# Performance work log

Measured on AMD Instinct MI355X. Metric: run time of the kernel, lower is better.

The kernel has to match this reference:

```python
import jax, jax.numpy as jnp
import numpy as np

N_BASIS = 5  # identity, transpose, diag-embed(diag), row-sum broadcast, total-sum broadcast


def eq2to2_ops(x):
    """x: [B, d, n, n] -> [B, 5, d, n, n] equivariant basis ops (sums normalized by n, n^2)."""
    n = x.shape[-1]
    eye = jnp.eye(n, dtype=x.dtype)
    xt = jnp.swapaxes(x, -1, -2)
    diag = jnp.diagonal(x, axis1=-2, axis2=-1)            # [B, d, n]
    diag_emb = diag[..., :, None] * eye                   # [B, d, n, n]
    row = jnp.broadcast_to(x.sum(-1, keepdims=True) / n, x.shape)
    tot = jnp.broadcast_to(x.sum((-2, -1), keepdims=True) / (n * n), x.shape)
    return jnp.stack([x, xt, diag_emb, row, tot], axis=1)


def eq_layer(x, W, b):
    """x: [B, d_in, n, n]; W: [d_in, d_out, 5]; b: [d_out] -> [B, d_out, n, n]."""
    ops = eq2to2_ops(x)                                   # [B, 5, d_in, n, n]
    return jnp.einsum('bqdij,dsq->bsij', ops, W) + b[None, :, None, None]


def setup_inputs() -> dict:
    key = jax.random.key(0)
    ks = jax.random.split(key, 8)
    B, n, nin, nhid, ndechid, nout = 8, 256, 16, 32, 128, 1
    s = lambda fan: 1.0 / np.sqrt(fan)
    return {
        'x': jax.random.normal(ks[0], (B, n, nin), jnp.float32),
        'W1': jax.random.normal(ks[1], (2 * nin, nhid, N_BASIS), jnp.float32) * s(2 * nin * N_BASIS),
        'b1': jnp.zeros((nhid,), jnp.float32),
        'W2': jax.random.normal(ks[2], (nhid, nhid, N_BASIS), jnp.float32) * s(nhid * N_BASIS),
        'b2': jnp.zeros((nhid,), jnp.float32),
        'D1': jax.random.normal(ks[3], (nhid, ndechid), jnp.float32) * s(nhid),
        'db1': jnp.zeros((ndechid,), jnp.float32),
        'D2': jax.random.normal(ks[4], (ndechid, ndechid), jnp.float32) * s(ndechid),
        'db2': jnp.zeros((ndechid,), jnp.float32),
        'D3': jax.random.normal(ks[5], (ndechid, nout), jnp.float32) * s(ndechid),
        'db3': jnp.zeros((nout,), jnp.float32),
    }


def reference(x, W1, b1, W2, b2, D1, db1, D2, db2, D3, db3):
    B, n, d = x.shape
    eye = jnp.eye(n, dtype=x.dtype)
    # diag_embed(x.permute(0,2,1)) -> [B, d, n, n]
    x1 = jnp.swapaxes(x, 1, 2)[..., :, None] * eye
    # outer-product pairwise interactions -> [B, d, n, n]
    x2 = jnp.einsum('bid,bjd->bdij', x, x)
    h = jnp.concatenate([x1, x2], axis=1)                 # [B, 2d, n, n]
    h = jax.nn.relu(eq_layer(h, W1, b1))
    h = jax.nn.relu(eq_layer(h, W2, b2))
    h = jax.nn.relu(h.sum((-2, -1)))                      # [B, nhid]
    h = jax.nn.relu(h @ D1 + db1)
    h = jax.nn.relu(h @ D2 + db2)
    return h @ D3 + db3
```

## Files before the change

### kernel.cpp

```cpp
#include <hip/hip_runtime.h>
#include <hip/hip_bf16.h>


#define NB 8
#define NN 256
#define ND 16
#define NC 32
#define W1S 160
#define W2S 160

using bf16x8 = __attribute__((ext_vector_type(8))) __bf16;
using f32x4  = __attribute__((ext_vector_type(4))) float;

#define MFMA(a, b, c) __builtin_amdgcn_mfma_f32_16x16x32_bf16((a), (b), (c), 0, 0, 0)

__global__ __launch_bounds__(256) void kC_rows(
    const float* __restrict__ x, const float* __restrict__ W1,
    const float* __restrict__ b1, const float* __restrict__ W2,
    float* __restrict__ T1g, float* __restrict__ R1, float* __restrict__ Dg1,
    float* __restrict__ TotP, float* __restrict__ CD2, float* __restrict__ CR2)
{
    const int TI = blockIdx.x, b = blockIdx.y, t = threadIdx.x;
    __shared__ __align__(16) float  sX[NN][ND + 1];
    __shared__ __align__(16) __bf16 sP[NN][40];
    __shared__ __align__(16) __bf16 sBQ[NC][48];
    __shared__ float part[16][ND + 1];
    __shared__ float sS[ND], sT1[NC];
    __shared__ float sRT[8][NC], sDgL[8][NC], sRow[8][NC], sDiag[8][NC];

    const float* xg = x + b * NN * ND;
    #pragma unroll
    for (int kk = 0; kk < 16; ++kk) {
        int idx = t + kk * 256;
        sX[idx >> 4][idx & 15] = xg[idx];
    }
    #pragma unroll
    for (int kk = 0; kk < 2; ++kk) {
        int idx = t + kk * 256;
        int c = idx >> 4, k = idx & 15;
        sBQ[c][k] = (__bf16)(W1[(ND + k) * W1S + c * 5 + 0]
                           + W1[(ND + k) * W1S + c * 5 + 1]);
    }
    #pragma unroll
    for (int kk = 0; kk < 4; ++kk) {
        int idx = t + kk * 256;
        sBQ[idx >> 5][16 + (idx & 31)] = (__bf16)0.f;
    }
    {
        uint32_t* z = (uint32_t*)&sP[0][0];
        #pragma unroll
        for (int kk = 0; kk < 8; ++kk) {
            int idx = t + kk * 256;
            z[(idx >> 3) * 20 + 8 + (idx & 7)] = 0u;
        }
    }
    __syncthreads();

    {
        int rr = t >> 4, d = t & 15;
        float p = 0.f;
        #pragma unroll
        for (int k = 0; k < 16; ++k) p += sX[rr + (k << 4)][d];
        part[rr][d] = p;
    }
    __syncthreads();
    if (t < ND) {
        float s = 0.f;
        #pragma unroll
        for (int k = 0; k < 16; ++k) s += part[k][t];
        sS[t] = s;
    }
    __syncthreads();
    if (t < NC) {
        int c = t; float tt = 0.f;
        #pragma unroll
        for (int d = 0; d < ND; ++d)
            tt += sS[d] * W1[d * W1S + c * 5 + 4]
                + sS[d] * sS[d] * W1[(ND + d) * W1S + c * 5 + 4];
        float v = tt * (1.f / 65536.f) + b1[c];
        sT1[c] = v;
        if (TI == 0) T1g[b * NC + c] = v;
    }
    __syncthreads();
    {
        int i_l = t >> 5, c = t & 31;
        int gi = TI * 8 + i_l;
        float r = 0.f, dg = 0.f;
        #pragma unroll
        for (int d = 0; d < ND; ++d) {
            float xi = sX[gi][d];
            const float* wa = W1 + d * W1S + c * 5;
            const float* wb = W1 + (ND + d) * W1S + c * 5;
            r  += xi * wa[3] + xi * sS[d] * wb[3];
            dg += xi * (wa[0] + wa[1] + wa[2]) + xi * xi * wb[2];
        }
        r *= (1.f / 256.f);
        R1[(b * NN + gi) * NC + c] = r;
        Dg1[(b * NN + gi) * NC + c] = dg;
        sRT[i_l][c] = sT1[c] + r;
        sDgL[i_l][c] = dg;
    }

    const int ln = t & 63, wv = t >> 6;
    const int m = ln & 15, quad = ln >> 4;
    bf16x8 bq0 = *(const bf16x8*)&sBQ[m][8 * quad];
    bf16x8 bq1 = *(const bf16x8*)&sBQ[m + 16][8 * quad];
    f32x4 zero = {0.f, 0.f, 0.f, 0.f};
    float rs0[4] = {0.f, 0.f, 0.f, 0.f}, rs1[4] = {0.f, 0.f, 0.f, 0.f};
    const int i_base = TI * 8;

    for (int jg = 0; jg < 8; ++jg) {
        __syncthreads();
        {
            int i_l = t >> 5, j_l = t & 31;
            const float* xi = &sX[i_base + i_l][0];
            const float* xj = &sX[jg * 32 + j_l][0];
            bf16x8 v0, v1;
            #pragma unroll
            for (int d = 0; d < 8; ++d) v0[d] = (__bf16)(xi[d] * xj[d]);
            #pragma unroll
            for (int d = 0; d < 8; ++d) v1[d] = (__bf16)(xi[8 + d] * xj[8 + d]);
            *(bf16x8*)&sP[t][0] = v0;
            *(bf16x8*)&sP[t][8] = v1;
        }
        __syncthreads();
        #pragma unroll
        for (int gg = 0; gg < 4; ++gg) {
            int g = wv * 4 + gg;
            bf16x8 av = *(const bf16x8*)&sP[g * 16 + m][8 * quad];
            f32x4 q0 = MFMA(av, bq0, zero);
            f32x4 q1 = MFMA(av, bq1, zero);
            int i_l = g >> 1;
            int gi = i_base + i_l;
            float rt0 = sRT[i_l][m], rt1 = sRT[i_l][m + 16];
            int jb = jg * 32 + (g & 1) * 16 + quad * 4;
            #pragma unroll
            for (int r = 0; r < 4; ++r) {
                float v0 = q0[r] + rt0, v1 = q1[r] + rt1;
                bool dgf = (jb + r == gi);
                if (dgf) { v0 += sDgL[i_l][m]; v1 += sDgL[i_l][m + 16]; }
                float h0 = fmaxf(v0, 0.f), h1 = fmaxf(v1, 0.f);
                if (dgf) { sDiag[i_l][m] = h0; sDiag[i_l][m + 16] = h1; }
                rs0[gg] += h0; rs1[gg] += h1;
            }
        }
    }
    float a0 = rs0[0] + rs0[1], a1 = rs0[2] + rs0[3];
    float b0 = rs1[0] + rs1[1], b1v = rs1[2] + rs1[3];
    a0 += __shfl_down(a0, 32, 64);  a0 += __shfl_down(a0, 16, 64);
    a1 += __shfl_down(a1, 32, 64);  a1 += __shfl_down(a1, 16, 64);
    b0 += __shfl_down(b0, 32, 64);  b0 += __shfl_down(b0, 16, 64);
    b1v += __shfl_down(b1v, 32, 64); b1v += __shfl_down(b1v, 16, 64);
    __syncthreads();
    if (ln < 16) {
        sRow[wv * 2][ln] = a0;       sRow[wv * 2 + 1][ln] = a1;
        sRow[wv * 2][ln + 16] = b0;  sRow[wv * 2 + 1][ln + 16] = b1v;
    }
    __syncthreads();
    if (t < NC) {
        float s = 0.f;
        #pragma unroll
        for (int i = 0; i < 8; ++i) s += sRow[i][t];
        TotP[TI * (NB * NC) + b * NC + t] = s;
    }
    {
        int i_l = t >> 5, s = t & 31;
        int gi = i_base + i_l;
        float cd = 0.f, cr = 0.f;
        #pragma unroll
        for (int c = 0; c < NC; ++c) {
            cd += sDiag[i_l][c] * W2[c * W2S + s * 5 + 2];
            cr += sRow[i_l][c]  * W2[c * W2S + s * 5 + 3];
        }
        CD2[(b * NN + gi) * NC + s] = cd;
        CR2[(b * NN + gi) * NC + s] = cr * (1.f / 256.f);
    }
}

__global__ __launch_bounds__(256) void kD_main(
    const float* __restrict__ x, const float* __restrict__ W1,
    const float* __restrict__ W2, const float* __restrict__ b2,
    const float* __restrict__ T1g, const float* __restrict__ R1g,
    const float* __restrict__ Dg1g, const float* __restrict__ CD2g,
    const float* __restrict__ CR2g, const float* __restrict__ TotP,
    float* __restrict__ GP)
{
    const int b = blockIdx.y, t = threadIdx.x;
    int TI = 0, rem = blockIdx.x;
    while (rem >= 16 - TI) { rem -= 16 - TI; ++TI; }
    const int TJ = TI + rem;
    const bool diagblk = (TI == TJ), mirror = !diagblk;

    __shared__ __align__(16) __bf16 sPA[NN][40];
    __shared__ __align__(16) __bf16 sV[NN][40];
    __shared__ __align__(16) __bf16 sBQ[NC][48];
    __shared__ __align__(16) __bf16 sWp[NC][40];
    __shared__ __align__(16) __bf16 sWm[NC][40];
    __shared__ float sXI[16][ND + 1], sXJ[16][ND + 1];
    __shared__ float sR1I[16][NC], sR1J[16][NC];
    __shared__ float sCR2I[16][NC], sCR2J[16][NC];
    __shared__ float sCD2I[16][NC], sDgI[16][NC];
    __shared__ float sT1[NC], sTot[NC], sCT2[NC];
    __shared__ float red[4][NC];

    { int r = t >> 4, d = t & 15;
      sXI[r][d] = x[(b * NN + TI * 16 + r) * ND + d];
      sXJ[r][d] = x[(b * NN + TJ * 16 + r) * ND + d]; }
    #pragma unroll
    for (int kk = 0; kk < 2; ++kk) {
      int idx = t + kk * 256; int r = idx >> 5, c = idx & 31;
      sR1I[r][c]  = R1g [(b * NN + TI * 16 + r) * NC + c];
      sR1J[r][c]  = R1g [(b * NN + TJ * 16 + r) * NC + c];
      sCR2I[r][c] = CR2g[(b * NN + TI * 16 + r) * NC + c];
      sCR2J[r][c] = CR2g[(b * NN + TJ * 16 + r) * NC + c];
      sCD2I[r][c] = CD2g[(b * NN + TI * 16 + r) * NC + c];
      sDgI[r][c]  = Dg1g[(b * NN + TI * 16 + r) * NC + c];
    }
    #pragma unroll
    for (int kk = 0; kk < 2; ++kk) {
      int idx = t + kk * 256; int c = idx >> 4, k = idx & 15;
      sBQ[c][k] = (__bf16)(W1[(ND + k) * W1S + c * 5 + 0]
                         + W1[(ND + k) * W1S + c * 5 + 1]);
    }
    #pragma unroll
    for (int kk = 0; kk < 4; ++kk) {
      int idx = t + kk * 256;
      sBQ[idx >> 5][16 + (idx & 31)] = (__bf16)0.f;
    }
    #pragma unroll
    for (int kk = 0; kk < 4; ++kk) {
      int idx = t + kk * 256; int s = idx >> 5, c = idx & 31;
      float w0 = W2[c * W2S + s * 5 + 0], w1 = W2[c * W2S + s * 5 + 1];
      sWp[s][c] = (__bf16)((w0 + w1) * 0.5f);
      sWm[s][c] = (__bf16)((w0 - w1) * 0.5f);
    }
    if (t < NC) {
      sT1[t] = T1g[b * NC + t];
      float tot = 0.f;
      #pragma unroll
      for (int k = 0; k < 32; ++k) tot += TotP[k * (NB * NC) + b * NC + t];
      sTot[t] = tot;
    }
    __syncthreads();

    {
      int ti = t >> 4, tj = t & 15;
      bf16x8 v0, v1, zv;
      #pragma unroll
      for (int d = 0; d < 8; ++d) {
        v0[d] = (__bf16)(sXI[ti][d] * sXJ[tj][d]);
        v1[d] = (__bf16)(sXI[ti][8 + d] * sXJ[tj][8 + d]);
        zv[d] = (__bf16)0.f;
      }
      *(bf16x8*)&sPA[t][0]  = v0;
      *(bf16x8*)&sPA[t][8]  = v1;
      *(bf16x8*)&sPA[t][16] = zv;
      *(bf16x8*)&sPA[t][24] = zv;
    }
    if (t < NC) {
      float ct = 0.f;
      #pragma unroll
      for (int c = 0; c < NC; ++c) ct += sTot[c] * W2[c * W2S + t * 5 + 4];
      sCT2[t] = ct * (1.f / 65536.f) + b2[t];
    }
    __syncthreads();

    const int wv = t >> 6, ln = t & 63;
    const int m = ln & 15, quad = ln >> 4;
    const int c0 = m, c1 = m + 16;
    f32x4 zero = {0.f, 0.f, 0.f, 0.f};

    {
      bf16x8 bq0 = *(const bf16x8*)&sBQ[c0][8 * quad];
      bf16x8 bq1 = *(const bf16x8*)&sBQ[c1][8 * quad];
      float t10 = sT1[c0], t11 = sT1[c1];
      #pragma unroll
      for (int gg = 0; gg < 4; ++gg) {
        int g = wv * 4 + gg;
        bf16x8 av = *(const bf16x8*)&sPA[g * 16 + m][8 * quad];
        f32x4 q0 = MFMA(av, bq0, zero);
        f32x4 q1 = MFMA(av, bq1, zero);
        float r1i0 = sR1I[g][c0] + t10, r1i1 = sR1I[g][c1] + t11;
        #pragma unroll
        for (int r = 0; r < 4; ++r) {
          int tj = quad * 4 + r;
          float a0 = q0[r] + r1i0, b0 = q0[r] + sR1J[tj][c0] + t10;
          float a1v = q1[r] + r1i1, b1v = q1[r] + sR1J[tj][c1] + t11;
          if (diagblk && tj == g) {
            a0 += sDgI[g][c0]; b0 = a0;
            a1v += sDgI[g][c1]; b1v = a1v;
          }
          float hA0 = fmaxf(a0, 0.f), hB0 = fmaxf(b0, 0.f);
          float hA1 = fmaxf(a1v, 0.f), hB1 = fmaxf(b1v, 0.f);
          int pos = g * 16 + tj;
          sPA[pos][c0] = (__bf16)(hA0 + hB0);  sV[pos][c0] = (__bf16)(hA0 - hB0);
          sPA[pos][c1] = (__bf16)(hA1 + hB1);  sV[pos][c1] = (__bf16)(hA1 - hB1);
        }
      }
    }
    __syncthreads();

    const int s0 = m, s1 = m + 16;
    bf16x8 wp0 = *(const bf16x8*)&sWp[s0][8 * quad];
    bf16x8 wp1 = *(const bf16x8*)&sWp[s1][8 * quad];
    bf16x8 wm0 = *(const bf16x8*)&sWm[s0][8 * quad];
    bf16x8 wm1 = *(const bf16x8*)&sWm[s1][8 * quad];
    float ct0 = sCT2[s0], ct1 = sCT2[s1];
    float acc0 = 0.f, acc1 = 0.f;
    #pragma unroll
    for (int gg = 0; gg < 4; ++gg) {
      int g = wv * 4 + gg;
      bf16x8 ua = *(const bf16x8*)&sPA[g * 16 + m][8 * quad];
      bf16x8 va = *(const bf16x8*)&sV [g * 16 + m][8 * quad];
      f32x4 P0 = MFMA(ua, wp0, zero);
      f32x4 M0 = MFMA(va, wm0, zero);
      f32x4 P1 = MFMA(ua, wp1, zero);
      f32x4 M1 = MFMA(va, wm1, zero);
      float crI0 = sCR2I[g][s0] + ct0, crI1 = sCR2I[g][s1] + ct1;
      float cd0 = sCD2I[g][s0], cd1 = sCD2I[g][s1];
      #pragma unroll
      for (int r = 0; r < 4; ++r) {
        int tj = quad * 4 + r;
        float a1 = P0[r] + M0[r] + crI0;
        float a2 = P0[r] - M0[r] + sCR2J[tj][s0] + ct0;
        float e1 = P1[r] + M1[r] + crI1;
        float e2 = P1[r] - M1[r] + sCR2J[tj][s1] + ct1;
        if (diagblk && tj == g) { a1 += cd0; e1 += cd1; }
        acc0 += fmaxf(a1, 0.f); acc1 += fmaxf(e1, 0.f);
        if (mirror) { acc0 += fmaxf(a2, 0.f); acc1 += fmaxf(e2, 0.f); }
      }
    }
    acc0 += __shfl_down(acc0, 32, 64); acc0 += __shfl_down(acc0, 16, 64);
    acc1 += __shfl_down(acc1, 32, 64); acc1 += __shfl_down(acc1, 16, 64);
    if (ln < 16) { red[wv][ln] = acc0; red[wv][ln + 16] = acc1; }
    __syncthreads();
    if (t < NC) {
      GP[blockIdx.x * (NB * NC) + b * NC + t]
          = red[0][t] + red[1][t] + red[2][t] + red[3][t];
    }
}

__global__ __launch_bounds__(128) void k5_mlp(
    const float* __restrict__ GP, const float* __restrict__ D1,
    const float* __restrict__ db1, const float* __restrict__ D2,
    const float* __restrict__ db2, const float* __restrict__ D3,
    const float* __restrict__ db3, float* __restrict__ out)
{
    int b = blockIdx.x, t = threadIdx.x;
    __shared__ float sGp[4][NC], a[NC], h2s[128], r2[2];
    {
        int q = t >> 5, s = t & 31;
        float p = 0.f;
        for (int k = q; k < 136; k += 4) p += GP[k * (NB * NC) + b * NC + s];
        sGp[q][s] = p;
    }
    __syncthreads();
    if (t < NC) a[t] = fmaxf(sGp[0][t] + sGp[1][t] + sGp[2][t] + sGp[3][t], 0.f);
    __syncthreads();
    float acc = db1[t];
    #pragma unroll
    for (int s = 0; s < NC; ++s) acc += a[s] * D1[s * 128 + t];
    float h2 = fmaxf(acc, 0.f);
    h2s[t] = h2;
    __syncthreads();
    float acc2 = db2[t];
    for (int u = 0; u < 128; ++u) acc2 += h2s[u] * D2[u * 128 + t];
    float h3 = fmaxf(acc2, 0.f);
    float v = h3 * D3[t];
    #pragma unroll
    for (int off = 32; off > 0; off >>= 1) v += __shfl_down(v, off, 64);
    if ((t & 63) == 0) r2[t >> 6] = v;
    __syncthreads();
    if (t == 0) out[b] = r2[0] + r2[1] + db3[0];
}

extern "C" void kernel_launch(void* const* d_in, const int* in_sizes, int n_in,
                              void* d_out, int out_size, void* d_ws, size_t ws_size,
                              hipStream_t stream)
{
    const float* x   = (const float*)d_in[0];
    const float* W1  = (const float*)d_in[1];
    const float* b1  = (const float*)d_in[2];
    const float* W2  = (const float*)d_in[3];
    const float* b2  = (const float*)d_in[4];
    const float* D1  = (const float*)d_in[5];
    const float* db1 = (const float*)d_in[6];
    const float* D2  = (const float*)d_in[7];
    const float* db2 = (const float*)d_in[8];
    const float* D3  = (const float*)d_in[9];
    const float* db3 = (const float*)d_in[10];
    float* out = (float*)d_out;

    float* w = (float*)d_ws;
    float* pT1   = w; w += NB * NC;
    float* pTotP = w; w += 32 * NB * NC;
    float* pGP   = w; w += 136 * NB * NC;
    float* pR1   = w; w += NB * NN * NC;
    float* pDg1  = w; w += NB * NN * NC;
    float* pCD2  = w; w += NB * NN * NC;
    float* pCR2  = w; w += NB * NN * NC;

    hipLaunchKernelGGL(kC_rows, dim3(32, NB), dim3(256), 0, stream,
                       x, W1, b1, W2, pT1, pR1, pDg1, pTotP, pCD2, pCR2);
    hipLaunchKernelGGL(kD_main, dim3(136, NB), dim3(256), 0, stream,
                       x, W1, W2, b2, pT1, pR1, pDg1, pCD2, pCR2, pTotP, pGP);
    hipLaunchKernelGGL(k5_mlp, dim3(NB), dim3(128), 0, stream,
                       pGP, D1, db1, D2, db2, D3, db3, out);
}
```

Measured before the change: 119.2 us.

## Build MFMA operands in registers and fuse MLP via last-block atomic reduction

The pairwise-product A operands for the MFMA calls are now built directly in registers from padded float rows of x, so the shared-memory staging buffer and its per-iteration barriers are gone. The separate MLP kernel is removed. kD_main atomically adds its per-block channel sums into a small per-batch accumulator, and the last block to finish for each batch, found with an atomic counter, runs the decoder MLP. This saves a kernel launch and the partial-sum buffer, at the cost of atomics, thread fences, and a float summation order that is no longer deterministic.

Result: slower. 165.0 us (+38.4%).

```diff
diff --git a/kernel.cpp b/kernel.cpp
--- a/kernel.cpp
+++ b/kernel.cpp
@@ -8,21 +8,40 @@
 #define NC 32
 #define W1S 160
 #define W2S 160
+#define XP 20
 
 using bf16x8 = __attribute__((ext_vector_type(8))) __bf16;
 using f32x4  = __attribute__((ext_vector_type(4))) float;
 
 #define MFMA(a, b, c) __builtin_amdgcn_mfma_f32_16x16x32_bf16((a), (b), (c), 0, 0, 0)
+
+__device__ __forceinline__ bf16x8 make_av(const float* xi, const float* xj, int quad)
+{
+    bf16x8 av;
+    if (quad < 2) {
+        const float4* a = (const float4*)(xi + quad * 8);
+        const float4* b = (const float4*)(xj + quad * 8);
+        float4 a0 = a[0], a1 = a[1], b0 = b[0], b1 = b[1];
+        av[0] = (__bf16)(a0.x * b0.x); av[1] = (__bf16)(a0.y * b0.y);
+        av[2] = (__bf16)(a0.z * b0.z); av[3] = (__bf16)(a0.w * b0.w);
+        av[4] = (__bf16)(a1.x * b1.x); av[5] = (__bf16)(a1.y * b1.y);
+        av[6] = (__bf16)(a1.z * b1.z); av[7] = (__bf16)(a1.w * b1.w);
+    } else {
+        #pragma unroll
+        for (int j = 0; j < 8; ++j) av[j] = (__bf16)0.f;
+    }
+    return av;
+}
 
 __global__ __launch_bounds__(256) void kC_rows(
     const float* __restrict__ x, const float* __restrict__ W1,
     const float* __restrict__ b1, const float* __restrict__ W2,
     float* __restrict__ T1g, float* __restrict__ R1, float* __restrict__ Dg1,
-    float* __restrict__ TotP, float* __restrict__ CD2, float* __restrict__ CR2)
+    float* __restrict__ TotP, float* __restrict__ CD2, float* __restrict__ CR2,
+    float* __restrict__ G, unsigned int* __restrict__ cnt)
 {
     const int TI = blockIdx.x, b = blockIdx.y, t = threadIdx.x;
-    __shared__ __align__(16) float  sX[NN][ND + 1];
-    __shared__ __align__(16) __bf16 sP[NN][40];
+    __shared__ __align__(16) float  sX[NN][XP];
     __shared__ __align__(16) __bf16 sBQ[NC][48];
     __shared__ float part[16][ND + 1];
     __shared__ float sS[ND], sT1[NC];
@@ -36,8 +55,7 @@
     }
     #pragma unroll
     for (int kk = 0; kk < 2; ++kk) {
-        int idx = t + kk * 256;
-        int c = idx >> 4, k = idx & 15;
+        int idx = t + kk * 256; int c = idx >> 4, k = idx & 15;
         sBQ[c][k] = (__bf16)(W1[(ND + k) * W1S + c * 5 + 0]
                            + W1[(ND + k) * W1S + c * 5 + 1]);
     }
@@ -46,13 +64,9 @@
         int idx = t + kk * 256;
         sBQ[idx >> 5][16 + (idx & 31)] = (__bf16)0.f;
     }
-    {
-        uint32_t* z = (uint32_t*)&sP[0][0];
-        #pragma unroll
-        for (int kk = 0; kk < 8; ++kk) {
-            int idx = t + kk * 256;
-            z[(idx >> 3) * 20 + 8 + (idx & 7)] = 0u;
-        }
+    if (TI == 0) {
+        if (t < NC) G[b * NC + t] = 0.f;
+        if (t == NC) cnt[b] = 0u;
     }
     __syncthreads();
 
@@ -100,6 +114,7 @@
         sRT[i_l][c] = sT1[c] + r;
         sDgL[i_l][c] = dg;
     }
+    __syncthreads();
 
     const int ln = t & 63, wv = t >> 6;
     const int m = ln & 15, quad = ln >> 4;
@@ -110,28 +125,15 @@
     const int i_base = TI * 8;
 
     for (int jg = 0; jg < 8; ++jg) {
-        __syncthreads();
-        {
-            int i_l = t >> 5, j_l = t & 31;
-            const float* xi = &sX[i_base + i_l][0];
-            const float* xj = &sX[jg * 32 + j_l][0];
-            bf16x8 v0, v1;
-            #pragma unroll
-            for (int d = 0; d < 8; ++d) v0[d] = (__bf16)(xi[d] * xj[d]);
-            #pragma unroll
-            for (int d = 0; d < 8; ++d) v1[d] = (__bf16)(xi[8 + d] * xj[8 + d]);
-            *(bf16x8*)&sP[t][0] = v0;
-            *(bf16x8*)&sP[t][8] = v1;
-        }
-        __syncthreads();
         #pragma unroll
         for (int gg = 0; gg < 4; ++gg) {
             int g = wv * 4 + gg;
-            bf16x8 av = *(const bf16x8*)&sP[g * 16 + m][8 * quad];
+            int i_l = g >> 1;
+            int gi = i_base + i_l;
+            int jrow = jg * 32 + (g & 1) * 16 + m;
+            bf16x8 av = make_av(&sX[gi][0], &sX[jrow][0], quad);
             f32x4 q0 = MFMA(av, bq0, zero);
             f32x4 q1 = MFMA(av, bq1, zero);
-            int i_l = g >> 1;
-            int gi = i_base + i_l;
             float rt0 = sRT[i_l][m], rt1 = sRT[i_l][m + 16];
             int jb = jg * 32 + (g & 1) * 16 + quad * 4;
             #pragma unroll
@@ -183,7 +185,11 @@
     const float* __restrict__ T1g, const float* __restrict__ R1g,
     const float* __restrict__ Dg1g, const float* __restrict__ CD2g,
     const float* __restrict__ CR2g, const float* __restrict__ TotP,
-    float* __restrict__ GP)
+    float* __restrict__ G, unsigned int* __restrict__ cnt,
+    const float* __restrict__ D1, const float* __restrict__ db1,
+    const float* __restrict__ D2, const float* __restrict__ db2,
+    const float* __restrict__ D3, const float* __restrict__ db3,
+    float* __restrict__ out)
 {
     const int b = blockIdx.y, t = threadIdx.x;
     int TI = 0, rem = blockIdx.x;
@@ -191,17 +197,19 @@
     const int TJ = TI + rem;
     const bool diagblk = (TI == TJ), mirror = !diagblk;
 
-    __shared__ __align__(16) __bf16 sPA[NN][40];
+    __shared__ __align__(16) __bf16 sU[NN][40];
     __shared__ __align__(16) __bf16 sV[NN][40];
     __shared__ __align__(16) __bf16 sBQ[NC][48];
     __shared__ __align__(16) __bf16 sWp[NC][40];
     __shared__ __align__(16) __bf16 sWm[NC][40];
-    __shared__ float sXI[16][ND + 1], sXJ[16][ND + 1];
+    __shared__ __align__(16) float sXI[16][XP], sXJ[16][XP];
     __shared__ float sR1I[16][NC], sR1J[16][NC];
     __shared__ float sCR2I[16][NC], sCR2J[16][NC];
     __shared__ float sCD2I[16][NC], sDgI[16][NC];
     __shared__ float sT1[NC], sTot[NC], sCT2[NC];
     __shared__ float red[4][NC];
+    __shared__ float mA[NC], mH[128], mR[2];
+    __shared__ bool  lastFlag;
 
     { int r = t >> 4, d = t & 15;
       sXI[r][d] = x[(b * NN + TI * 16 + r) * ND + d];
@@ -242,61 +250,47 @@
       sTot[t] = tot;
     }
     __syncthreads();
-
-    {
-      int ti = t >> 4, tj = t & 15;
-      bf16x8 v0, v1, zv;
-      #pragma unroll
-      for (int d = 0; d < 8; ++d) {
-        v0[d] = (__bf16)(sXI[ti][d] * sXJ[tj][d]);
-        v1[d] = (__bf16)(sXI[ti][8 + d] * sXJ[tj][8 + d]);
-        zv[d] = (__bf16)0.f;
-      }
-      *(bf16x8*)&sPA[t][0]  = v0;
-      *(bf16x8*)&sPA[t][8]  = v1;
-      *(bf16x8*)&sPA[t][16] = zv;
-      *(bf16x8*)&sPA[t][24] = zv;
-    }
     if (t < NC) {
       float ct = 0.f;
       #pragma unroll
       for (int c = 0; c < NC; ++c) ct += sTot[c] * W2[c * W2S + t * 5 + 4];
       sCT2[t] = ct * (1.f / 65536.f) + b2[t];
     }
-    __syncthreads();
-
-    const int wv = t >> 6, ln = t & 63;
+
+    const int ln = t & 63, wv = t >> 6;
     const int m = ln & 15, quad = ln >> 4;
     const int c0 = m, c1 = m + 16;
     f32x4 zero = {0.f, 0.f, 0.f, 0.f};
 
     {
-      bf16x8 bq0 = *(const bf16x8*)&sBQ[c0][8 * quad];
-      bf16x8 bq1 = *(const bf16x8*)&sBQ[c1][8 * quad];
-      float t10 = sT1[c0], t11 = sT1[c1];
-      #pragma unroll
-      for (int gg = 0; gg < 4; ++gg) {
-        int g = wv * 4 + gg;
-        bf16x8 av = *(const bf16x8*)&sPA[g * 16 + m][8 * quad];
-        f32x4 q0 = MFMA(av, bq0, zero);
-        f32x4 q1 = MFMA(av, bq1, zero);
-        float r1i0 = sR1I[g][c0] + t10, r1i1 = sR1I[g][c1] + t11;
-        #pragma unroll
-        for (int r = 0; r < 4; ++r) {
-          int tj = quad * 4 + r;
-          float a0 = q0[r] + r1i0, b0 = q0[r] + sR1J[tj][c0] + t10;
-          float a1v = q1[r] + r1i1, b1v = q1[r] + sR1J[tj][c1] + t11;
-          if (diagblk && tj == g) {
-            a0 += sDgI[g][c0]; b0 = a0;
-            a1v += sDgI[g][c1]; b1v = a1v;
-          }
-          float hA0 = fmaxf(a0, 0.f), hB0 = fmaxf(b0, 0.f);
-          float hA1 = fmaxf(a1v, 0.f), hB1 = fmaxf(b1v, 0.f);
-          int pos = g * 16 + tj;
-          sPA[pos][c0] = (__bf16)(hA0 + hB0);  sV[pos][c0] = (__bf16)(hA0 - hB0);
-          sPA[pos][c1] = (__bf16)(hA1 + hB1);  sV[pos][c1] = (__bf16)(hA1 - hB1);
+        bf16x8 bq0 = *(const bf16x8*)&sBQ[c0][8 * quad];
+        bf16x8 bq1 = *(const bf16x8*)&sBQ[c1][8 * quad];
+        float t10 = sT1[c0], t11 = sT1[c1];
+        #pragma unroll
+        for (int gg = 0; gg < 4; ++gg) {
+            int g = wv * 4 + gg;
+            bf16x8 av = make_av(&sXI[g][0], &sXJ[m][0], quad);
+            f32x4 q0 = MFMA(av, bq0, zero);
+            f32x4 q1 = MFMA(av, bq1, zero);
+            float r1i0 = sR1I[g][c0] + t10, r1i1 = sR1I[g][c1] + t11;
+            #pragma unroll
+            for (int r = 0; r < 4; ++r) {
+                int tj = quad * 4 + r;
+                float a0 = q0[r] + r1i0, b0 = q0[r] + sR1J[tj][c0] + t10;
+                float a1v = q1[r] + r1i1, b1v = q1[r] + sR1J[tj][c1] + t11;
+                if (diagblk && tj == g) {
+                    a0 += sDgI[g][c0]; b0 = a0;
+                    a1v += sDgI[g][c1]; b1v = a1v;
+                }
+                float hA0 = fmaxf(a0, 0.f), hB0 = fmaxf(b0, 0.f);
+                float hA1 = fmaxf(a1v, 0.f), hB1 = fmaxf(b1v, 0.f);
+                int pos = g * 16 + tj;
+                sU[pos][c0] = (__bf16)(hA0 + hB0);
+                sV[pos][c0] = (__bf16)(hA0 - hB0);
+                sU[pos][c1] = (__bf16)(hA1 + hB1);
+                sV[pos][c1] = (__bf16)(hA1 - hB1);
+            }
         }
-      }
     }
     __syncthreads();
 
@@ -309,69 +303,67 @@
     float acc0 = 0.f, acc1 = 0.f;
     #pragma unroll
     for (int gg = 0; gg < 4; ++gg) {
-      int g = wv * 4 + gg;
-      bf16x8 ua = *(const bf16x8*)&sPA[g * 16 + m][8 * quad];
-      bf16x8 va = *(const bf16x8*)&sV [g * 16 + m][8 * quad];
-      f32x4 P0 = MFMA(ua, wp0, zero);
-      f32x4 M0 = MFMA(va, wm0, zero);
-      f32x4 P1 = MFMA(ua, wp1, zero);
-      f32x4 M1 = MFMA(va, wm1, zero);
-      float crI0 = sCR2I[g][s0] + ct0, crI1 = sCR2I[g][s1] + ct1;
-      float cd0 = sCD2I[g][s0], cd1 = sCD2I[g][s1];
-      #pragma unroll
-      for (int r = 0; r < 4; ++r) {
-        int tj = quad * 4 + r;
-        float a1 = P0[r] + M0[r] + crI0;
-        float a2 = P0[r] - M0[r] + sCR2J[tj][s0] + ct0;
-        float e1 = P1[r] + M1[r] + crI1;
-        float e2 = P1[r] - M1[r] + sCR2J[tj][s1] + ct1;
-        if (diagblk && tj == g) { a1 += cd0; e1 += cd1; }
-        acc0 += fmaxf(a1, 0.f); acc1 += fmaxf(e1, 0.f);
-        if (mirror) { acc0 += fmaxf(a2, 0.f); acc1 += fmaxf(e2, 0.f); }
-      }
+        int g = wv * 4 + gg;
+        bf16x8 ua = *(const bf16x8*)&sU[g * 16 + m][8 * quad];
+        bf16x8 va = *(const bf16x8*)&sV[g * 16 + m][8 * quad];
+        f32x4 P0 = MFMA(ua, wp0, zero);
+        f32x4 M0 = MFMA(va, wm0, zero);
+        f32x4 P1 = MFMA(ua, wp1, zero);
+        f32x4 M1 = MFMA(va, wm1, zero);
+        float crI0 = sCR2I[g][s0] + ct0, crI1 = sCR2I[g][s1] + ct1;
+        float cd0 = sCD2I[g][s0], cd1 = sCD2I[g][s1];
+        #pragma unroll
+        for (int r = 0; r < 4; ++r) {
+            int tj = quad * 4 + r;
+            float a1 = P0[r] + M0[r] + crI0;
+            float a2 = P0[r] - M0[r] + sCR2J[tj][s0] + ct0;
+            float e1 = P1[r] + M1[r] + crI1;
+            float e2 = P1[r] - M1[r] + sCR2J[tj][s1] + ct1;
+            if (diagblk && tj == g) { a1 += cd0; e1 += cd1; }
+            acc0 += fmaxf(a1, 0.f); acc1 += fmaxf(e1, 0.f);
+            if (mirror) { acc0 += fmaxf(a2, 0.f); acc1 += fmaxf(e2, 0.f); }
+        }
     }
     acc0 += __shfl_down(acc0, 32, 64); acc0 += __shfl_down(acc0, 16, 64);
     acc1 += __shfl_down(acc1, 32, 64); acc1 += __shfl_down(acc1, 16, 64);
+    __syncthreads();
     if (ln < 16) { red[wv][ln] = acc0; red[wv][ln + 16] = acc1; }
     __syncthreads();
-    if (t < NC) {
-      GP[blockIdx.x * (NB * NC) + b * NC + t]
-          = red[0][t] + red[1][t] + red[2][t] + red[3][t];
-    }
-}
-
-__global__ __launch_bounds__(128) void k5_mlp(
-    const float* __restrict__ GP, const float* __restrict__ D1,
-    const float* __restrict__ db1, const float* __restrict__ D2,
-    const float* __restrict__ db2, const float* __restrict__ D3,
-    const float* __restrict__ db3, float* __restrict__ out)
-{
-    int b = blockIdx.x, t = threadIdx.x;
-    __shared__ float sGp[4][NC], a[NC], h2s[128], r2[2];
-    {
-        int q = t >> 5, s = t & 31;
-        float p = 0.f;
-        for (int k = q; k < 136; k += 4) p += GP[k * (NB * NC) + b * NC + s];
-        sGp[q][s] = p;
-    }
-    __syncthreads();
-    if (t < NC) a[t] = fmaxf(sGp[0][t] + sGp[1][t] + sGp[2][t] + sGp[3][t], 0.f);
-    __syncthreads();
-    float acc = db1[t];
-    #pragma unroll
-    for (int s = 0; s < NC; ++s) acc += a[s] * D1[s * 128 + t];
-    float h2 = fmaxf(acc, 0.f);
-    h2s[t] = h2;
-    __syncthreads();
-    float acc2 = db2[t];
-    for (int u = 0; u < 128; ++u) acc2 += h2s[u] * D2[u * 128 + t];
-    float h3 = fmaxf(acc2, 0.f);
-    float v = h3 * D3[t];
-    #pragma unroll
-    for (int off = 32; off > 0; off >>= 1) v += __shfl_down(v, off, 64);
-    if ((t & 63) == 0) r2[t >> 6] = v;
-    __syncthreads();
-    if (t == 0) out[b] = r2[0] + r2[1] + db3[0];
+    if (t < NC)
+        atomicAdd(&G[b * NC + t], red[0][t] + red[1][t] + red[2][t] + red[3][t]);
+
+    __threadfence();
+    if (t == 0) {
+        unsigned int old = atomicAdd(&cnt[b], 1u);
+        lastFlag = (old == 135u);
+    }
+    __syncthreads();
+    if (!lastFlag) return;
+    __threadfence();
+
+    if (t < NC)
+        mA[t] = fmaxf(__hip_atomic_load(&G[b * NC + t], __ATOMIC_RELAXED,
+                                        __HIP_MEMORY_SCOPE_AGENT), 0.f);
+    __syncthreads();
+    if (t < 128) {
+        float acc = db1[t];
+        #pragma unroll
+        for (int s = 0; s < NC; ++s) acc += mA[s] * D1[s * 128 + t];
+        mH[t] = fmaxf(acc, 0.f);
+    }
+    __syncthreads();
+    if (t < 128) {
+        float acc2 = db2[t];
+        #pragma unroll 8
+        for (int u = 0; u < 128; ++u) acc2 += mH[u] * D2[u * 128 + t];
+        float h3 = fmaxf(acc2, 0.f);
+        float v = h3 * D3[t];
+        #pragma unroll
+        for (int off = 32; off > 0; off >>= 1) v += __shfl_down(v, off, 64);
+        if ((t & 63) == 0) mR[t >> 6] = v;
+    }
+    __syncthreads();
+    if (t == 0) out[b] = mR[0] + mR[1] + db3[0];
 }
 
 extern "C" void kernel_launch(void* const* d_in, const int* in_sizes, int n_in,
@@ -394,16 +386,17 @@
     float* w = (float*)d_ws;
     float* pT1   = w; w += NB * NC;
     float* pTotP = w; w += 32 * NB * NC;
-    float* pGP   = w; w += 136 * NB * NC;
+    float* pG    = w; w += NB * NC;
+    unsigned int* pCnt = (unsigned int*)w; w += NB;
     float* pR1   = w; w += NB * NN * NC;
     float* pDg1  = w; w += NB * NN * NC;
     float* pCD2  = w; w += NB * NN * NC;
     float* pCR2  = w; w += NB * NN * NC;
 
     hipLaunchKernelGGL(kC_rows, dim3(32, NB), dim3(256), 0, stream,
-                       x, W1, b1, W2, pT1, pR1, pDg1, pTotP, pCD2, pCR2);
+                       x, W1, b1, W2, pT1, pR1, pDg1, pTotP, pCD2, pCR2,
+                       pG, pCnt);
     hipLaunchKernelGGL(kD_main, dim3(136, NB), dim3(256), 0, stream,
-                       x, W1, W2, b2, pT1, pR1, pDg1, pCD2, pCR2, pTotP, pGP);
-    hipLaunchKernelGGL(k5_mlp, dim3(NB), dim3(128), 0, stream,
-                       pGP, D1, db1, D2, db2, D3, db3, out);
+                       x, W1, W2, b2, pT1, pR1, pDg1, pCD2, pCR2, pTotP,
+                       pG, pCnt, D1, db1, D2, db2, D3, db3, out);
 }
```

## Build MFMA operands in registers and use per-wave LDS staging with wave-level sync

Applied to the files above, without the earlier changes.

The pairwise-product A operands are now built directly in registers from the x rows, which removes the shared product buffers and the block-wide barriers around them. In the second stage each wave stages its U/V tiles in a private LDS slice and syncs with a wave barrier and waitcnt instead of __syncthreads. Per-row constants move from LDS into registers, and the row kernel doubles its grid so each block handles 4 rows. The W2 K-dimension is permuted to match the packed bf16 pair writes, and the waitcnt-based wave sync relies on an encoding-specific immediate.

Measured after the change: 115.5 us. 3.1% less time.

```diff
diff --git a/kernel.cpp b/kernel.cpp
--- a/kernel.cpp
+++ b/kernel.cpp
@@ -8,11 +8,43 @@
 #define NC 32
 #define W1S 160
 #define W2S 160
+#define XP 20
 
 using bf16x8 = __attribute__((ext_vector_type(8))) __bf16;
 using f32x4  = __attribute__((ext_vector_type(4))) float;
 
 #define MFMA(a, b, c) __builtin_amdgcn_mfma_f32_16x16x32_bf16((a), (b), (c), 0, 0, 0)
+
+#define WAVE_LDS_SYNC() do {                      \
+    __builtin_amdgcn_wave_barrier();              \
+    __builtin_amdgcn_s_waitcnt(0xc07f);  \
+    __builtin_amdgcn_wave_barrier();              \
+} while (0)
+
+__device__ __forceinline__ bf16x8 make_av(const float* xi, const float* xj, int quad)
+{
+    bf16x8 av;
+    if (quad < 2) {
+        const float4* a = (const float4*)(xi + quad * 8);
+        const float4* b = (const float4*)(xj + quad * 8);
+        float4 a0 = a[0], a1 = a[1], b0 = b[0], b1 = b[1];
+        av[0] = (__bf16)(a0.x * b0.x); av[1] = (__bf16)(a0.y * b0.y);
+        av[2] = (__bf16)(a0.z * b0.z); av[3] = (__bf16)(a0.w * b0.w);
+        av[4] = (__bf16)(a1.x * b1.x); av[5] = (__bf16)(a1.y * b1.y);
+        av[6] = (__bf16)(a1.z * b1.z); av[7] = (__bf16)(a1.w * b1.w);
+    } else {
+        #pragma unroll
+        for (int j = 0; j < 8; ++j) av[j] = (__bf16)0.f;
+    }
+    return av;
+}
+
+__device__ __forceinline__ unsigned pack2(float lo, float hi)
+{
+    union { __bf16 b[2]; unsigned u; } p;
+    p.b[0] = (__bf16)lo; p.b[1] = (__bf16)hi;
+    return p.u;
+}
 
 __global__ __launch_bounds__(256) void kC_rows(
     const float* __restrict__ x, const float* __restrict__ W1,
@@ -21,12 +53,11 @@
     float* __restrict__ TotP, float* __restrict__ CD2, float* __restrict__ CR2)
 {
     const int TI = blockIdx.x, b = blockIdx.y, t = threadIdx.x;
-    __shared__ __align__(16) float  sX[NN][ND + 1];
-    __shared__ __align__(16) __bf16 sP[NN][40];
+    __shared__ __align__(16) float  sX[NN][XP];
     __shared__ __align__(16) __bf16 sBQ[NC][48];
     __shared__ float part[16][ND + 1];
     __shared__ float sS[ND], sT1[NC];
-    __shared__ float sRT[8][NC], sDgL[8][NC], sRow[8][NC], sDiag[8][NC];
+    __shared__ float sRT[4][NC], sDgL[4][NC], sRow[4][NC], sDiag[4][NC];
 
     const float* xg = x + b * NN * ND;
     #pragma unroll
@@ -36,8 +67,7 @@
     }
     #pragma unroll
     for (int kk = 0; kk < 2; ++kk) {
-        int idx = t + kk * 256;
-        int c = idx >> 4, k = idx & 15;
+        int idx = t + kk * 256; int c = idx >> 4, k = idx & 15;
         sBQ[c][k] = (__bf16)(W1[(ND + k) * W1S + c * 5 + 0]
                            + W1[(ND + k) * W1S + c * 5 + 1]);
     }
@@ -45,14 +75,6 @@
     for (int kk = 0; kk < 4; ++kk) {
         int idx = t + kk * 256;
         sBQ[idx >> 5][16 + (idx & 31)] = (__bf16)0.f;
-    }
-    {
-        uint32_t* z = (uint32_t*)&sP[0][0];
-        #pragma unroll
-        for (int kk = 0; kk < 8; ++kk) {
-            int idx = t + kk * 256;
-            z[(idx >> 3) * 20 + 8 + (idx & 7)] = 0u;
-        }
     }
     __syncthreads();
 
@@ -82,9 +104,9 @@
         if (TI == 0) T1g[b * NC + c] = v;
     }
     __syncthreads();
-    {
+    if (t < 128) {
         int i_l = t >> 5, c = t & 31;
-        int gi = TI * 8 + i_l;
+        int gi = TI * 4 + i_l;
         float r = 0.f, dg = 0.f;
         #pragma unroll
         for (int d = 0; d < ND; ++d) {
@@ -100,80 +122,55 @@
         sRT[i_l][c] = sT1[c] + r;
         sDgL[i_l][c] = dg;
     }
+    __syncthreads();
 
     const int ln = t & 63, wv = t >> 6;
     const int m = ln & 15, quad = ln >> 4;
+    const int gi = TI * 4 + wv;
     bf16x8 bq0 = *(const bf16x8*)&sBQ[m][8 * quad];
     bf16x8 bq1 = *(const bf16x8*)&sBQ[m + 16][8 * quad];
+    float rt0 = sRT[wv][m], rt1 = sRT[wv][m + 16];
+    float dg0 = sDgL[wv][m], dg1 = sDgL[wv][m + 16];
     f32x4 zero = {0.f, 0.f, 0.f, 0.f};
-    float rs0[4] = {0.f, 0.f, 0.f, 0.f}, rs1[4] = {0.f, 0.f, 0.f, 0.f};
-    const int i_base = TI * 8;
+    float rs0 = 0.f, rs1 = 0.f;
 
     for (int jg = 0; jg < 8; ++jg) {
-        __syncthreads();
-        {
-            int i_l = t >> 5, j_l = t & 31;
-            const float* xi = &sX[i_base + i_l][0];
-            const float* xj = &sX[jg * 32 + j_l][0];
-            bf16x8 v0, v1;
-            #pragma unroll
-            for (int d = 0; d < 8; ++d) v0[d] = (__bf16)(xi[d] * xj[d]);
-            #pragma unroll
-            for (int d = 0; d < 8; ++d) v1[d] = (__bf16)(xi[8 + d] * xj[8 + d]);
-            *(bf16x8*)&sP[t][0] = v0;
-            *(bf16x8*)&sP[t][8] = v1;
-        }
-        __syncthreads();
-        #pragma unroll
-        for (int gg = 0; gg < 4; ++gg) {
-            int g = wv * 4 + gg;
-            bf16x8 av = *(const bf16x8*)&sP[g * 16 + m][8 * quad];
+        #pragma unroll
+        for (int gg = 0; gg < 2; ++gg) {
+            int jrow = jg * 32 + gg * 16 + m;
+            bf16x8 av = make_av(&sX[gi][0], &sX[jrow][0], quad);
             f32x4 q0 = MFMA(av, bq0, zero);
             f32x4 q1 = MFMA(av, bq1, zero);
-            int i_l = g >> 1;
-            int gi = i_base + i_l;
-            float rt0 = sRT[i_l][m], rt1 = sRT[i_l][m + 16];
-            int jb = jg * 32 + (g & 1) * 16 + quad * 4;
+            int jb = jg * 32 + gg * 16 + quad * 4;
             #pragma unroll
             for (int r = 0; r < 4; ++r) {
                 float v0 = q0[r] + rt0, v1 = q1[r] + rt1;
                 bool dgf = (jb + r == gi);
-                if (dgf) { v0 += sDgL[i_l][m]; v1 += sDgL[i_l][m + 16]; }
+                if (dgf) { v0 += dg0; v1 += dg1; }
                 float h0 = fmaxf(v0, 0.f), h1 = fmaxf(v1, 0.f);
-                if (dgf) { sDiag[i_l][m] = h0; sDiag[i_l][m + 16] = h1; }
-                rs0[gg] += h0; rs1[gg] += h1;
+                if (dgf) { sDiag[wv][m] = h0; sDiag[wv][m + 16] = h1; }
+                rs0 += h0; rs1 += h1;
             }
         }
     }
-    float a0 = rs0[0] + rs0[1], a1 = rs0[2] + rs0[3];
-    float b0 = rs1[0] + rs1[1], b1v = rs1[2] + rs1[3];
-    a0 += __shfl_down(a0, 32, 64);  a0 += __shfl_down(a0, 16, 64);
-    a1 += __shfl_down(a1, 32, 64);  a1 += __shfl_down(a1, 16, 64);
-    b0 += __shfl_down(b0, 32, 64);  b0 += __shfl_down(b0, 16, 64);
-    b1v += __shfl_down(b1v, 32, 64); b1v += __shfl_down(b1v, 16, 64);
-    __syncthreads();
-    if (ln < 16) {
-        sRow[wv * 2][ln] = a0;       sRow[wv * 2 + 1][ln] = a1;
-        sRow[wv * 2][ln + 16] = b0;  sRow[wv * 2 + 1][ln + 16] = b1v;
-    }
-    __syncthreads();
-    if (t < NC) {
-        float s = 0.f;
-        #pragma unroll
-        for (int i = 0; i < 8; ++i) s += sRow[i][t];
-        TotP[TI * (NB * NC) + b * NC + t] = s;
-    }
-    {
+    rs0 += __shfl_down(rs0, 32, 64); rs0 += __shfl_down(rs0, 16, 64);
+    rs1 += __shfl_down(rs1, 32, 64); rs1 += __shfl_down(rs1, 16, 64);
+    if (ln < 16) { sRow[wv][ln] = rs0; sRow[wv][ln + 16] = rs1; }
+    __syncthreads();
+    if (t < NC)
+        TotP[TI * (NB * NC) + b * NC + t]
+            = sRow[0][t] + sRow[1][t] + sRow[2][t] + sRow[3][t];
+    if (t < 128) {
         int i_l = t >> 5, s = t & 31;
-        int gi = i_base + i_l;
+        int gi2 = TI * 4 + i_l;
         float cd = 0.f, cr = 0.f;
         #pragma unroll
         for (int c = 0; c < NC; ++c) {
             cd += sDiag[i_l][c] * W2[c * W2S + s * 5 + 2];
             cr += sRow[i_l][c]  * W2[c * W2S + s * 5 + 3];
         }
-        CD2[(b * NN + gi) * NC + s] = cd;
-        CR2[(b * NN + gi) * NC + s] = cr * (1.f / 256.f);
+        CD2[(b * NN + gi2) * NC + s] = cd;
+        CR2[(b * NN + gi2) * NC + s] = cr * (1.f / 256.f);
     }
 }
 
@@ -191,153 +188,158 @@
     const int TJ = TI + rem;
     const bool diagblk = (TI == TJ), mirror = !diagblk;
 
-    __shared__ __align__(16) __bf16 sPA[NN][40];
-    __shared__ __align__(16) __bf16 sV[NN][40];
+    __shared__ __align__(16) __bf16 sUw[4][16][40];
+    __shared__ __align__(16) __bf16 sVw[4][16][40];
     __shared__ __align__(16) __bf16 sBQ[NC][48];
-    __shared__ __align__(16) __bf16 sWp[NC][40];
-    __shared__ __align__(16) __bf16 sWm[NC][40];
-    __shared__ float sXI[16][ND + 1], sXJ[16][ND + 1];
-    __shared__ float sR1I[16][NC], sR1J[16][NC];
-    __shared__ float sCR2I[16][NC], sCR2J[16][NC];
-    __shared__ float sCD2I[16][NC], sDgI[16][NC];
-    __shared__ float sT1[NC], sTot[NC], sCT2[NC];
+    __shared__ __align__(16) __bf16 sWp[NC][40], sWm[NC][40];
+    __shared__ __align__(16) float sXI[16][XP], sXJ[16][XP];
+    __shared__ float sTot[NC], sCT2[NC];
     __shared__ float red[4][NC];
 
-    { int r = t >> 4, d = t & 15;
-      sXI[r][d] = x[(b * NN + TI * 16 + r) * ND + d];
-      sXJ[r][d] = x[(b * NN + TJ * 16 + r) * ND + d]; }
     #pragma unroll
     for (int kk = 0; kk < 2; ++kk) {
-      int idx = t + kk * 256; int r = idx >> 5, c = idx & 31;
-      sR1I[r][c]  = R1g [(b * NN + TI * 16 + r) * NC + c];
-      sR1J[r][c]  = R1g [(b * NN + TJ * 16 + r) * NC + c];
-      sCR2I[r][c] = CR2g[(b * NN + TI * 16 + r) * NC + c];
-      sCR2J[r][c] = CR2g[(b * NN + TJ * 16 + r) * NC + c];
-      sCD2I[r][c] = CD2g[(b * NN + TI * 16 + r) * NC + c];
-      sDgI[r][c]  = Dg1g[(b * NN + TI * 16 + r) * NC + c];
+        int idx = t + kk * 256; int rr = idx >> 4, d = idx & 15;
+        if (rr < 16) sXI[rr][d] = x[(b * NN + TI * 16 + rr) * ND + d];
+        else         sXJ[rr - 16][d] = x[(b * NN + TJ * 16 + rr - 16) * ND + d];
     }
     #pragma unroll
     for (int kk = 0; kk < 2; ++kk) {
-      int idx = t + kk * 256; int c = idx >> 4, k = idx & 15;
-      sBQ[c][k] = (__bf16)(W1[(ND + k) * W1S + c * 5 + 0]
-                         + W1[(ND + k) * W1S + c * 5 + 1]);
+        int idx = t + kk * 256; int c = idx >> 4, k = idx & 15;
+        sBQ[c][k] = (__bf16)(W1[(ND + k) * W1S + c * 5 + 0]
+                           + W1[(ND + k) * W1S + c * 5 + 1]);
     }
     #pragma unroll
     for (int kk = 0; kk < 4; ++kk) {
-      int idx = t + kk * 256;
-      sBQ[idx >> 5][16 + (idx & 31)] = (__bf16)0.f;
+        int idx = t + kk * 256;
+        sBQ[idx >> 5][16 + (idx & 31)] = (__bf16)0.f;
     }
     #pragma unroll
     for (int kk = 0; kk < 4; ++kk) {
-      int idx = t + kk * 256; int s = idx >> 5, c = idx & 31;
-      float w0 = W2[c * W2S + s * 5 + 0], w1 = W2[c * W2S + s * 5 + 1];
-      sWp[s][c] = (__bf16)((w0 + w1) * 0.5f);
-      sWm[s][c] = (__bf16)((w0 - w1) * 0.5f);
+        int idx = t + kk * 256; int s = idx >> 5, kp = idx & 31;
+        int c = ((kp & 1) << 4) | (kp >> 1);
+        float w0 = W2[c * W2S + s * 5 + 0], w1 = W2[c * W2S + s * 5 + 1];
+        sWp[s][kp] = (__bf16)((w0 + w1) * 0.5f);
+        sWm[s][kp] = (__bf16)((w0 - w1) * 0.5f);
     }
     if (t < NC) {
-      sT1[t] = T1g[b * NC + t];
-      float tot = 0.f;
-      #pragma unroll
-      for (int k = 0; k < 32; ++k) tot += TotP[k * (NB * NC) + b * NC + t];
-      sTot[t] = tot;
-    }
-    __syncthreads();
-
-    {
-      int ti = t >> 4, tj = t & 15;
-      bf16x8 v0, v1, zv;
-      #pragma unroll
-      for (int d = 0; d < 8; ++d) {
-        v0[d] = (__bf16)(sXI[ti][d] * sXJ[tj][d]);
-        v1[d] = (__bf16)(sXI[ti][8 + d] * sXJ[tj][8 + d]);
-        zv[d] = (__bf16)0.f;
-      }
-      *(bf16x8*)&sPA[t][0]  = v0;
-      *(bf16x8*)&sPA[t][8]  = v1;
-      *(bf16x8*)&sPA[t][16] = zv;
-      *(bf16x8*)&sPA[t][24] = zv;
-    }
+        float tot = 0.f;
+        #pragma unroll
+        for (int k = 0; k < 64; ++k) tot += TotP[k * (NB * NC) + b * NC + t];
+        sTot[t] = tot;
+    }
+
+    const int ln = t & 63, wv = t >> 6;
+    const int m = ln & 15, quad = ln >> 4;
+
+    const float* R1b = R1g + b * NN * NC;
+    const float* Dgb = Dg1g + b * NN * NC;
+    const float* CDb = CD2g + b * NN * NC;
+    const float* CRb = CR2g + b * NN * NC;
+    float t10 = T1g[b * NC + m], t11 = T1g[b * NC + m + 16];
+    float rti[4][2], dgi[4][2], rtj[4][2];
+    #pragma unroll
+    for (int gg = 0; gg < 4; ++gg) {
+        int rowI = TI * 16 + wv * 4 + gg;
+        rti[gg][0] = R1b[rowI * NC + m] + t10;
+        rti[gg][1] = R1b[rowI * NC + m + 16] + t11;
+        dgi[gg][0] = Dgb[rowI * NC + m];
+        dgi[gg][1] = Dgb[rowI * NC + m + 16];
+    }
+    #pragma unroll
+    for (int r = 0; r < 4; ++r) {
+        int rowJ = TJ * 16 + quad * 4 + r;
+        rtj[r][0] = R1b[rowJ * NC + m] + t10;
+        rtj[r][1] = R1b[rowJ * NC + m + 16] + t11;
+    }
+    __syncthreads();
     if (t < NC) {
-      float ct = 0.f;
-      #pragma unroll
-      for (int c = 0; c < NC; ++c) ct += sTot[c] * W2[c * W2S + t * 5 + 4];
-      sCT2[t] = ct * (1.f / 65536.f) + b2[t];
-    }
-    __syncthreads();
-
-    const int wv = t >> 6, ln = t & 63;
-    const int m = ln & 15, quad = ln >> 4;
-    const int c0 = m, c1 = m + 16;
+        float ct = 0.f;
+        #pragma unroll
+        for (int c = 0; c < NC; ++c) ct += sTot[c] * W2[c * W2S + t * 5 + 4];
+        sCT2[t] = ct * (1.f / 65536.f) + b2[t];
+    }
+    __syncthreads();
+
+    float ct0 = sCT2[m], ct1 = sCT2[m + 16];
+    float cri[4][2], cdi[4][2], crj[4][2];
+    #pragma unroll
+    for (int gg = 0; gg < 4; ++gg) {
+        int rowI = TI * 16 + wv * 4 + gg;
+        cri[gg][0] = CRb[rowI * NC + m] + ct0;
+        cri[gg][1] = CRb[rowI * NC + m + 16] + ct1;
+        cdi[gg][0] = CDb[rowI * NC + m];
+        cdi[gg][1] = CDb[rowI * NC + m + 16];
+    }
+    #pragma unroll
+    for (int r = 0; r < 4; ++r) {
+        int rowJ = TJ * 16 + quad * 4 + r;
+        crj[r][0] = CRb[rowJ * NC + m] + ct0;
+        crj[r][1] = CRb[rowJ * NC + m + 16] + ct1;
+    }
+
+    bf16x8 bq0 = *(const bf16x8*)&sBQ[m][8 * quad];
+    bf16x8 bq1 = *(const bf16x8*)&sBQ[m + 16][8 * quad];
+    bf16x8 wp0 = *(const bf16x8*)&sWp[m][8 * quad];
+    bf16x8 wp1 = *(const bf16x8*)&sWp[m + 16][8 * quad];
+    bf16x8 wm0 = *(const bf16x8*)&sWm[m][8 * quad];
+    bf16x8 wm1 = *(const bf16x8*)&sWm[m + 16][8 * quad];
+    __bf16* Uw = &sUw[wv][0][0];
+    __bf16* Vw = &sVw[wv][0][0];
     f32x4 zero = {0.f, 0.f, 0.f, 0.f};
-
-    {
-      bf16x8 bq0 = *(const bf16x8*)&sBQ[c0][8 * quad];
-      bf16x8 bq1 = *(const bf16x8*)&sBQ[c1][8 * quad];
-      float t10 = sT1[c0], t11 = sT1[c1];
-      #pragma unroll
-      for (int gg = 0; gg < 4; ++gg) {
+    float acc0 = 0.f, acc1 = 0.f;
+
+    #pragma unroll
+    for (int gg = 0; gg < 4; ++gg) {
         int g = wv * 4 + gg;
-        bf16x8 av = *(const bf16x8*)&sPA[g * 16 + m][8 * quad];
-        f32x4 q0 = MFMA(av, bq0, zero);
-        f32x4 q1 = MFMA(av, bq1, zero);
-        float r1i0 = sR1I[g][c0] + t10, r1i1 = sR1I[g][c1] + t11;
-        #pragma unroll
-        for (int r = 0; r < 4; ++r) {
-          int tj = quad * 4 + r;
-          float a0 = q0[r] + r1i0, b0 = q0[r] + sR1J[tj][c0] + t10;
-          float a1v = q1[r] + r1i1, b1v = q1[r] + sR1J[tj][c1] + t11;
-          if (diagblk && tj == g) {
-            a0 += sDgI[g][c0]; b0 = a0;
-            a1v += sDgI[g][c1]; b1v = a1v;
-          }
-          float hA0 = fmaxf(a0, 0.f), hB0 = fmaxf(b0, 0.f);
-          float hA1 = fmaxf(a1v, 0.f), hB1 = fmaxf(b1v, 0.f);
-          int pos = g * 16 + tj;
-          sPA[pos][c0] = (__bf16)(hA0 + hB0);  sV[pos][c0] = (__bf16)(hA0 - hB0);
-          sPA[pos][c1] = (__bf16)(hA1 + hB1);  sV[pos][c1] = (__bf16)(hA1 - hB1);
+        __builtin_amdgcn_wave_barrier();
+        {
+            bf16x8 av = make_av(&sXI[g][0], &sXJ[m][0], quad);
+            f32x4 q0 = MFMA(av, bq0, zero);
+            f32x4 q1 = MFMA(av, bq1, zero);
+            #pragma unroll
+            for (int r = 0; r < 4; ++r) {
+                int tj = quad * 4 + r;
+                float a0 = q0[r] + rti[gg][0], b0 = q0[r] + rtj[r][0];
+                float a1 = q1[r] + rti[gg][1], b1 = q1[r] + rtj[r][1];
+                if (diagblk && tj == g) {
+                    a0 += dgi[gg][0]; b0 = a0;
+                    a1 += dgi[gg][1]; b1 = a1;
+                }
+                float hA0 = fmaxf(a0, 0.f), hB0 = fmaxf(b0, 0.f);
+                float hA1 = fmaxf(a1, 0.f), hB1 = fmaxf(b1, 0.f);
+                *(unsigned*)&Uw[tj * 40 + 2 * m] = pack2(hA0 + hB0, hA1 + hB1);
+                *(unsigned*)&Vw[tj * 40 + 2 * m] = pack2(hA0 - hB0, hA1 - hB1);
+            }
         }
-      }
-    }
-    __syncthreads();
-
-    const int s0 = m, s1 = m + 16;
-    bf16x8 wp0 = *(const bf16x8*)&sWp[s0][8 * quad];
-    bf16x8 wp1 = *(const bf16x8*)&sWp[s1][8 * quad];
-    bf16x8 wm0 = *(const bf16x8*)&sWm[s0][8 * quad];
-    bf16x8 wm1 = *(const bf16x8*)&sWm[s1][8 * quad];
-    float ct0 = sCT2[s0], ct1 = sCT2[s1];
-    float acc0 = 0.f, acc1 = 0.f;
-    #pragma unroll
-    for (int gg = 0; gg < 4; ++gg) {
-      int g = wv * 4 + gg;
-      bf16x8 ua = *(const bf16x8*)&sPA[g * 16 + m][8 * quad];
-      bf16x8 va = *(const bf16x8*)&sV [g * 16 + m][8 * quad];
-      f32x4 P0 = MFMA(ua, wp0, zero);
-      f32x4 M0 = MFMA(va, wm0, zero);
-      f32x4 P1 = MFMA(ua, wp1, zero);
-      f32x4 M1 = MFMA(va, wm1, zero);
-      float crI0 = sCR2I[g][s0] + ct0, crI1 = sCR2I[g][s1] + ct1;
-      float cd0 = sCD2I[g][s0], cd1 = sCD2I[g][s1];
-      #pragma unroll
-      for (int r = 0; r < 4; ++r) {
-        int tj = quad * 4 + r;
-        float a1 = P0[r] + M0[r] + crI0;
-        float a2 = P0[r] - M0[r] + sCR2J[tj][s0] + ct0;
-        float e1 = P1[r] + M1[r] + crI1;
-        float e2 = P1[r] - M1[r] + sCR2J[tj][s1] + ct1;
-        if (diagblk && tj == g) { a1 += cd0; e1 += cd1; }
-        acc0 += fmaxf(a1, 0.f); acc1 += fmaxf(e1, 0.f);
-        if (mirror) { acc0 += fmaxf(a2, 0.f); acc1 += fmaxf(e2, 0.f); }
-      }
-    }
+        WAVE_LDS_SYNC();
+        {
+            bf16x8 ua = *(const bf16x8*)&Uw[m * 40 + 8 * quad];
+            bf16x8 va = *(const bf16x8*)&Vw[m * 40 + 8 * quad];
+            f32x4 P0 = MFMA(ua, wp0, zero);
+            f32x4 M0 = MFMA(va, wm0, zero);
+            f32x4 P1 = MFMA(ua, wp1, zero);
+            f32x4 M1 = MFMA(va, wm1, zero);
+            #pragma unroll
+            for (int r = 0; r < 4; ++r) {
+                int tj = quad * 4 + r;
+                float a1v = P0[r] + M0[r] + cri[gg][0];
+                float a2v = P0[r] - M0[r] + crj[r][0];
+                float e1 = P1[r] + M1[r] + cri[gg][1];
+                float e2 = P1[r] - M1[r] + crj[r][1];
+                if (diagblk && tj == g) { a1v += cdi[gg][0]; e1 += cdi[gg][1]; }
+                acc0 += fmaxf(a1v, 0.f); acc1 += fmaxf(e1, 0.f);
+                if (mirror) { acc0 += fmaxf(a2v, 0.f); acc1 += fmaxf(e2, 0.f); }
+            }
+        }
+    }
+
     acc0 += __shfl_down(acc0, 32, 64); acc0 += __shfl_down(acc0, 16, 64);
     acc1 += __shfl_down(acc1, 32, 64); acc1 += __shfl_down(acc1, 16, 64);
     if (ln < 16) { red[wv][ln] = acc0; red[wv][ln + 16] = acc1; }
     __syncthreads();
-    if (t < NC) {
-      GP[blockIdx.x * (NB * NC) + b * NC + t]
-          = red[0][t] + red[1][t] + red[2][t] + red[3][t];
-    }
+    if (t < NC)
+        GP[blockIdx.x * (NB * NC) + b * NC + t]
+            = red[0][t] + red[1][t] + red[2][t] + red[3][t];
 }
 
 __global__ __launch_bounds__(128) void k5_mlp(
@@ -364,6 +366,7 @@
     h2s[t] = h2;
     __syncthreads();
     float acc2 = db2[t];
+    #pragma unroll 8
     for (int u = 0; u < 128; ++u) acc2 += h2s[u] * D2[u * 128 + t];
     float h3 = fmaxf(acc2, 0.f);
     float v = h3 * D3[t];
@@ -393,14 +396,14 @@
 
     float* w = (float*)d_ws;
     float* pT1   = w; w += NB * NC;
-    float* pTotP = w; w += 32 * NB * NC;
+    float* pTotP = w; w += 64 * NB * NC;
     float* pGP   = w; w += 136 * NB * NC;
     float* pR1   = w; w += NB * NN * NC;
     float* pDg1  = w; w += NB * NN * NC;
     float* pCD2  = w; w += NB * NN * NC;
     float* pCR2  = w; w += NB * NN * NC;
 
-    hipLaunchKernelGGL(kC_rows, dim3(32, NB), dim3(256), 0, stream,
+    hipLaunchKernelGGL(kC_rows, dim3(64, NB), dim3(256), 0, stream,
                        x, W1, b1, W2, pT1, pR1, pDg1, pTotP, pCD2, pCR2);
     hipLaunchKernelGGL(kD_main, dim3(136, NB), dim3(256), 0, stream,
                        x, W1, W2, b2, pT1, pR1, pDg1, pCD2, pCR2, pTotP, pGP);
```
